# Performance work log

Measured on AMD Instinct MI355X. Metric: run time of the kernel, lower is better.

The kernel has to match this reference:

```python
import jax, jax.numpy as jnp
import numpy as np
import math

NUM_HEADS = 8

def setup_inputs() -> dict:
    key = jax.random.key(0)
    k1, k2, k3 = jax.random.split(key, 3)
    B, N, C = 16, 4096, 512
    x = jax.random.normal(k1, (B, N, C), dtype=jnp.float32)
    qkv_w = jax.random.normal(k2, (3 * C, C), dtype=jnp.float32) * 0.02
    proj_w = jax.random.normal(k3, (C, C), dtype=jnp.float32) * 0.02
    proj_b = jnp.zeros((C,), dtype=jnp.float32)
    return {"x": x, "qkv_w": qkv_w, "proj_w": proj_w, "proj_b": proj_b}


def reference(x, qkv_w, proj_w, proj_b):
    # Attention with is_mask=1: row-wise windowed attention.
    B, N, C = x.shape
    H = W = int(math.isqrt(N))
    nh = NUM_HEADS
    hd = C // nh
    scale = hd ** (-0.5)

    # fold rows into batch: (B*H, W, C)
    img = x.reshape(B * H, W, C)
    # qkv linear (no bias): (B*H, W, 3C) -> (3, B*H, nh, W, hd)
    qkv = jnp.einsum('bwc,dc->bwd', img, qkv_w)
    qkv = qkv.reshape(B * H, W, 3, nh, hd).transpose(2, 0, 3, 1, 4)
    q, k, v = qkv[0], qkv[1], qkv[2]

    # scaled dot-product attention within each row window
    attn = jnp.einsum('bhqd,bhkd->bhqk', q, k) * scale
    attn = jax.nn.softmax(attn, axis=-1)
    out = jnp.einsum('bhqk,bhkd->bhqd', attn, v)   # (B*H, nh, W, hd)
    out = out.transpose(0, 2, 1, 3).reshape(B, N, C)

    # output projection
    return jnp.einsum('bnc,dc->bnd', out, proj_w) + proj_b
```

## Files before the change

kernel.cpp:

```cpp
#include <hip/hip_runtime.h>
#include <cstdint>
#include <cstddef>

typedef _Float16 half8 __attribute__((ext_vector_type(8)));
typedef _Float16 half4 __attribute__((ext_vector_type(4)));
typedef float f32x4 __attribute__((ext_vector_type(4)));

#define GLDS16(g, l) __builtin_amdgcn_global_load_lds( \
    (__attribute__((address_space(1))) void*)(g), \
    (__attribute__((address_space(3))) void*)(l), 16, 0, 0)

__global__ __launch_bounds__(256) void cvt_f32_f16(const float* __restrict__ src,
                                                   _Float16* __restrict__ dst, int n) {
  int i = (blockIdx.x * 256 + threadIdx.x) * 8;
  if (i >= n) return;
  float4 a = *(const float4*)(src + i);
  float4 b = *(const float4*)(src + i + 4);
  half8 h;
  h[0] = (_Float16)a.x; h[1] = (_Float16)a.y; h[2] = (_Float16)a.z; h[3] = (_Float16)a.w;
  h[4] = (_Float16)b.x; h[5] = (_Float16)b.y; h[6] = (_Float16)b.z; h[7] = (_Float16)b.w;
  *(half8*)(dst + i) = h;
}

template<int NOUT, int NT, bool BIAS>
__global__ __launch_bounds__(256, 3) void gemm_bt(const _Float16* __restrict__ A,
                                                  const _Float16* __restrict__ Bw,
                                                  const float* __restrict__ bias,
                                                  void* __restrict__ Cout) {
  constexpr int K = 512;
  __shared__ union {
    struct { _Float16 As[4096]; _Float16 Bs[4096]; } s;
    float E[2][16][132];
  } u;
  const int id  = blockIdx.x;
  const int xcd = id & 7;
  const int jj  = id >> 3;
  const int by  = (jj / NT) * 8 + xcd;
  const int bx  = jj % NT;
  const int m_base = by * 128, n_base = bx * 128;

  const int t    = threadIdx.x;
  const int lane = t & 63;
  const int wid  = t >> 6;
  const int wm   = wid >> 1, wn = wid & 1;
  const int cl   = lane & 15, q = lane >> 4;

  f32x4 acc[4][4] = {};

  const int s0 = t, s1 = t + 256;
  const int r0 = ((s0 >> 6) << 4) | (s0 & 15), c0 = (s0 >> 4) & 3;
  const int r1 = ((s1 >> 6) << 4) | (s1 & 15), c1 = (s1 >> 4) & 3;
  const _Float16* a0 = A  + (size_t)(m_base + r0) * K + c0 * 8;
  const _Float16* a1 = A  + (size_t)(m_base + r1) * K + c1 * 8;
  const _Float16* b0 = Bw + (size_t)(n_base + r0) * K + c0 * 8;
  const _Float16* b1 = Bw + (size_t)(n_base + r1) * K + c1 * 8;
  char* adst0 = (char*)u.s.As + s0 * 16;
  char* adst1 = (char*)u.s.As + s1 * 16;
  char* bdst0 = (char*)u.s.Bs + s0 * 16;
  char* bdst1 = (char*)u.s.Bs + s1 * 16;

  const int lane8 = lane * 8;

  for (int k0 = 0; k0 < K; k0 += 32) {
    GLDS16(a0 + k0, adst0);
    GLDS16(a1 + k0, adst1);
    GLDS16(b0 + k0, bdst0);
    GLDS16(b1 + k0, bdst1);
    __syncthreads();
    half8 af[4], bf[4];
#pragma unroll
    for (int i = 0; i < 4; i++) af[i] = *(const half8*)(u.s.As + (wm * 4 + i) * 512 + lane8);
#pragma unroll
    for (int i = 0; i < 4; i++) bf[i] = *(const half8*)(u.s.Bs + (wn * 4 + i) * 512 + lane8);
#pragma unroll
    for (int mt = 0; mt < 4; mt++)
#pragma unroll
      for (int nt = 0; nt < 4; nt++)
        acc[mt][nt] = __builtin_amdgcn_mfma_f32_16x16x32_f16(af[mt], bf[nt], acc[mt][nt], 0, 0, 0);
    __syncthreads();
  }

  const int ebnd = t >> 7, erow = (t >> 3) & 15, ecs = t & 7;
#pragma unroll
  for (int mt = 0; mt < 4; mt++) {
#pragma unroll
    for (int nt = 0; nt < 4; nt++)
#pragma unroll
      for (int r = 0; r < 4; r++)
        u.E[wm][q * 4 + r][wn * 64 + nt * 16 + cl] = acc[mt][nt][r];
    __syncthreads();
    const size_t rg = (size_t)(m_base + ebnd * 64 + mt * 16 + erow);
#pragma unroll
    for (int j = 0; j < 4; j++) {
      const int ch = ((ecs - erow) & 7) + 8 * j;
      const int cc = ch * 4;
      float4 e = *(const float4*)&u.E[ebnd][erow][cc];
      if constexpr (BIAS) {
        const float4 bb = *(const float4*)(bias + n_base + cc);
        e.x += bb.x; e.y += bb.y; e.z += bb.z; e.w += bb.w;
        *(float4*)((float*)Cout + rg * NOUT + n_base + cc) = e;
      } else {
        half4 hv;
        hv[0] = (_Float16)e.x; hv[1] = (_Float16)e.y;
        hv[2] = (_Float16)e.z; hv[3] = (_Float16)e.w;
        *(half4*)((_Float16*)Cout + rg * NOUT + n_base + cc) = hv;
      }
    }
    __syncthreads();
  }
}

__global__ __launch_bounds__(256, 3) void attn_win(const _Float16* __restrict__ QKV,
                                                   _Float16* __restrict__ Out) {
  __shared__ _Float16 Qs[4096];
  __shared__ _Float16 Ks[4096];
  __shared__ _Float16 Vt[64][72];
  __shared__ _Float16 Ps[64][72];
  __shared__ _Float16 Os[64][72];
  const int h = blockIdx.x, b = blockIdx.y;
  const int t = threadIdx.x;
  const int lane = t & 63, wid = t >> 6;
  const int cl = lane & 15, q = lane >> 4;

  {
    const int s0 = t, s1 = t + 256;
    const int r0 = ((s0 >> 7) << 4) | (s0 & 15), ch0 = (s0 >> 4) & 7;
    const int r1 = ((s1 >> 7) << 4) | (s1 & 15), ch1 = (s1 >> 4) & 7;
    const _Float16* g0 = QKV + (size_t)(b * 64 + r0) * 1536 + h * 64 + ch0 * 8;
    const _Float16* g1 = QKV + (size_t)(b * 64 + r1) * 1536 + h * 64 + ch1 * 8;
    GLDS16(g0,       (char*)Qs + s0 * 16);
    GLDS16(g1,       (char*)Qs + s1 * 16);
    GLDS16(g0 + 512, (char*)Ks + s0 * 16);
    GLDS16(g1 + 512, (char*)Ks + s1 * 16);

    const int vj = t & 63, vp = t >> 6;
    const _Float16* vsrc = QKV + (size_t)(b * 64 + vj) * 1536 + 1024 + h * 64 + vp * 16;
    half8 v0 = *(const half8*)vsrc;
    half8 v1 = *(const half8*)(vsrc + 8);
#pragma unroll
    for (int i = 0; i < 8; i++) Vt[vp * 16 + i][vj] = v0[i];
#pragma unroll
    for (int i = 0; i < 8; i++) Vt[vp * 16 + 8 + i][vj] = v1[i];
  }
  __syncthreads();

  const int m0 = wid * 16;
  const int lane8 = lane * 8;

  f32x4 s[4] = {};
#pragma unroll
  for (int ks = 0; ks < 2; ks++) {
    half8 a = *(const half8*)(Qs + wid * 1024 + ks * 512 + lane8);
#pragma unroll
    for (int nt = 0; nt < 4; nt++) {
      half8 bb = *(const half8*)(Ks + nt * 1024 + ks * 512 + lane8);
      s[nt] = __builtin_amdgcn_mfma_f32_16x16x32_f16(a, bb, s[nt], 0, 0, 0);
    }
  }

  constexpr float SC = 0.125f * 1.44269504088896340736f;
#pragma unroll
  for (int r = 0; r < 4; r++) {
    float mx = fmaxf(fmaxf(s[0][r], s[1][r]), fmaxf(s[2][r], s[3][r]));
    mx = fmaxf(mx, __shfl_xor(mx, 1));
    mx = fmaxf(mx, __shfl_xor(mx, 2));
    mx = fmaxf(mx, __shfl_xor(mx, 4));
    mx = fmaxf(mx, __shfl_xor(mx, 8));
    float e[4], ssum = 0.f;
#pragma unroll
    for (int nt = 0; nt < 4; nt++) { e[nt] = exp2f((s[nt][r] - mx) * SC); ssum += e[nt]; }
    ssum += __shfl_xor(ssum, 1);
    ssum += __shfl_xor(ssum, 2);
    ssum += __shfl_xor(ssum, 4);
    ssum += __shfl_xor(ssum, 8);
    float inv = 1.f / ssum;
    const int row = m0 + q * 4 + r;
#pragma unroll
    for (int nt = 0; nt < 4; nt++) Ps[row][nt * 16 + cl] = (_Float16)(e[nt] * inv);
  }
  __syncthreads();

  f32x4 o[4] = {};
#pragma unroll
  for (int ks = 0; ks < 2; ks++) {
    half8 a = *(const half8*)&Ps[m0 + cl][ks * 32 + q * 8];
#pragma unroll
    for (int nt = 0; nt < 4; nt++) {
      half8 bb = *(const half8*)&Vt[nt * 16 + cl][ks * 32 + q * 8];
      o[nt] = __builtin_amdgcn_mfma_f32_16x16x32_f16(a, bb, o[nt], 0, 0, 0);
    }
  }
#pragma unroll
  for (int nt = 0; nt < 4; nt++)
#pragma unroll
    for (int r = 0; r < 4; r++)
      Os[m0 + q * 4 + r][nt * 16 + cl] = (_Float16)o[nt][r];
  __syncthreads();

  {
    const int row = t >> 2, cs = t & 3;
    half8 h0 = *(const half8*)&Os[row][cs * 16];
    half8 h1 = *(const half8*)&Os[row][cs * 16 + 8];
    _Float16* dst = Out + (size_t)(b * 64 + row) * 512 + h * 64 + cs * 16;
    *(half8*)dst = h0;
    *((half8*)dst + 1) = h1;
  }
}

extern "C" void kernel_launch(void* const* d_in, const int* in_sizes, int n_in,
                              void* d_out, int out_size, void* d_ws, size_t ws_size,
                              hipStream_t stream) {
  const float* x      = (const float*)d_in[0];
  const float* qkv_w  = (const float*)d_in[1];
  const float* proj_w = (const float*)d_in[2];
  const float* proj_b = (const float*)d_in[3];
  float* out = (float*)d_out;

  char* ws = (char*)d_ws;
  _Float16* QKVh = (_Float16*)ws;
  _Float16* Xh   = (_Float16*)(ws + 201326592);
  _Float16* Outh = Xh;
  _Float16* Wq   = (_Float16*)(ws + 268435456);
  _Float16* Wp   = (_Float16*)(ws + 270008320);

  cvt_f32_f16<<<16384, 256, 0, stream>>>(x, Xh, 16 * 4096 * 512);
  cvt_f32_f16<<<384, 256, 0, stream>>>(qkv_w, Wq, 1536 * 512);
  cvt_f32_f16<<<128, 256, 0, stream>>>(proj_w, Wp, 512 * 512);
  gemm_bt<1536, 12, false><<<6144, 256, 0, stream>>>(Xh, Wq, nullptr, QKVh);
  attn_win<<<dim3(8, 1024), 256, 0, stream>>>(QKVh, Outh);
  gemm_bt<512, 4, true><<<2048, 256, 0, stream>>>(Outh, Wp, proj_b, out);
}
```

Measured before the change: 580.3 us.

## Triple-buffer GEMM shared-memory tiles with async global-to-LDS prefetch

The GEMM K-loop now cycles through three LDS stages and issues global_load_lds copies two iterations ahead. It uses explicit vmcnt waits and a single barrier per iteration in place of two syncthreads. The goal is to hide global memory latency behind MFMA work and cut barrier stalls. LDS use grows from 16KB to 48KB per block, which may lower occupancy below the three blocks per CU the launch bounds target.

```diff
diff --git a/kernel.cpp b/kernel.cpp
--- a/kernel.cpp
+++ b/kernel.cpp
@@ -28,8 +28,9 @@
                                                   const float* __restrict__ bias,
                                                   void* __restrict__ Cout) {
   constexpr int K = 512;
+  constexpr int NIT = K / 32;
   __shared__ union {
-    struct { _Float16 As[4096]; _Float16 Bs[4096]; } s;
+    _Float16 S[3][2][4096];
     float E[2][16][132];
   } u;
   const int id  = blockIdx.x;
@@ -54,31 +55,42 @@
   const _Float16* a1 = A  + (size_t)(m_base + r1) * K + c1 * 8;
   const _Float16* b0 = Bw + (size_t)(n_base + r0) * K + c0 * 8;
   const _Float16* b1 = Bw + (size_t)(n_base + r1) * K + c1 * 8;
-  char* adst0 = (char*)u.s.As + s0 * 16;
-  char* adst1 = (char*)u.s.As + s1 * 16;
-  char* bdst0 = (char*)u.s.Bs + s0 * 16;
-  char* bdst1 = (char*)u.s.Bs + s1 * 16;
 
   const int lane8 = lane * 8;
 
-  for (int k0 = 0; k0 < K; k0 += 32) {
-    GLDS16(a0 + k0, adst0);
-    GLDS16(a1 + k0, adst1);
-    GLDS16(b0 + k0, bdst0);
-    GLDS16(b1 + k0, bdst1);
-    __syncthreads();
+  auto stage = [&](int kt, int b) {
+    const int ko = kt * 32;
+    GLDS16(a0 + ko, (char*)&u.S[b][0][0] + s0 * 16);
+    GLDS16(a1 + ko, (char*)&u.S[b][0][0] + s1 * 16);
+    GLDS16(b0 + ko, (char*)&u.S[b][1][0] + s0 * 16);
+    GLDS16(b1 + ko, (char*)&u.S[b][1][0] + s1 * 16);
+  };
+
+  stage(0, 0);
+  stage(1, 1);
+
+#pragma unroll
+  for (int k = 0; k < NIT; ++k) {
+    if (k < NIT - 1) asm volatile("s_waitcnt vmcnt(4)" ::: "memory");
+    else             asm volatile("s_waitcnt vmcnt(0)" ::: "memory");
+    __builtin_amdgcn_s_barrier();
+    asm volatile("" ::: "memory");
+    if (k < NIT - 2) stage(k + 2, (k + 2) % 3);
+
+    const _Float16* As = &u.S[k % 3][0][0];
+    const _Float16* Bs = &u.S[k % 3][1][0];
     half8 af[4], bf[4];
 #pragma unroll
-    for (int i = 0; i < 4; i++) af[i] = *(const half8*)(u.s.As + (wm * 4 + i) * 512 + lane8);
-#pragma unroll
-    for (int i = 0; i < 4; i++) bf[i] = *(const half8*)(u.s.Bs + (wn * 4 + i) * 512 + lane8);
+    for (int i = 0; i < 4; i++) af[i] = *(const half8*)(As + (wm * 4 + i) * 512 + lane8);
+#pragma unroll
+    for (int i = 0; i < 4; i++) bf[i] = *(const half8*)(Bs + (wn * 4 + i) * 512 + lane8);
 #pragma unroll
     for (int mt = 0; mt < 4; mt++)
 #pragma unroll
       for (int nt = 0; nt < 4; nt++)
         acc[mt][nt] = __builtin_amdgcn_mfma_f32_16x16x32_f16(af[mt], bf[nt], acc[mt][nt], 0, 0, 0);
-    __syncthreads();
-  }
+  }
+  __syncthreads();
 
   const int ebnd = t >> 7, erow = (t >> 3) & 15, ecs = t & 7;
 #pragma unroll
```

New measurement: 531.5 us. 8.4% less time.
